# Kernel tuning notes

Hardware: AMD Instinct MI355X
Metric: run time of the kernel (lower is better)

The kernel has to match this reference:

```python
import jax, jax.numpy as jnp
import numpy as np
from jax.ops import segment_sum

N_NODES = 100000
N_EDGES = 3200000
DIM = 256
N_CLASSES = 32
N_GRAPHS = 64


def setup_inputs() -> dict:
    key = jax.random.key(0)
    k1, k2, k3, k4, k5 = jax.random.split(key, 5)
    x = jax.random.normal(k1, (N_NODES, DIM), dtype=jnp.float32)
    W = jax.random.normal(k2, (DIM, N_CLASSES), dtype=jnp.float32) / np.sqrt(DIM)
    b = jax.random.normal(k3, (N_CLASSES,), dtype=jnp.float32) * 0.01
    edge_index = jax.random.randint(k4, (2, N_EDGES), 0, N_NODES, dtype=jnp.int64)
    batch = jnp.sort(jax.random.randint(k5, (N_NODES,), 0, N_GRAPHS, dtype=jnp.int64))
    return {"x": x, "W": W, "b": b, "edge_index": edge_index, "batch": batch}


def reference(x, W, b, edge_index, batch):
    N = x.shape[0]
    # GCNConv: linear transform (no bias), then normalized aggregation, then bias
    h = x @ W  # [N, C]
    # add self loops (PyG default add_self_loops=True)
    loop = jnp.arange(N, dtype=edge_index.dtype)
    src = jnp.concatenate([edge_index[0], loop])  # source (message sender)
    dst = jnp.concatenate([edge_index[1], loop])  # target (aggregation site)
    # symmetric normalization: deg computed at target with unit edge weights
    deg = segment_sum(jnp.ones_like(dst, dtype=h.dtype), dst, num_segments=N)
    dinv = jnp.where(deg > 0, jax.lax.rsqrt(deg), 0.0)
    norm = dinv[src] * dinv[dst]  # [E+N]
    msg = h[src] * norm[:, None]  # gather + scale
    out = segment_sum(msg, dst, num_segments=N) + b  # scatter-add, bias after agg
    # global_mean_pool: segment mean over graphs
    cnt = segment_sum(jnp.ones((N,), dtype=out.dtype), batch, num_segments=N_GRAPHS)
    sums = segment_sum(out, batch, num_segments=N_GRAPHS)
    return sums / jnp.maximum(cnt, 1.0)[:, None]
```

## Files before the change

### kernel.cpp

```cpp
#include <hip/hip_runtime.h>

#define NN    100000
#define NE    3200000
#define DIMK  256
#define NC    32
#define NG    64

#define ROWS   64
#define NBUCK  1563
#define CAP    2432
#define NB1    512
#define EPB    6250
#define NSL    16
#define MAXG   512

static constexpr size_t OFF_REC    = 0;
static constexpr size_t OFF_DINV   = 15204864;
static constexpr size_t OFF_BTOT   = 15604864;
static constexpr size_t OFF_START  = 15613056;
static constexpr size_t OFF_CTRL   = 15613568;
static constexpr size_t OFF_P2     = 15613696;
static constexpr size_t OFF_PART   = 16662272;
static constexpr size_t OFF_DEGARR = OFF_PART;
static constexpr size_t OFF_CNT    = OFF_PART + 400000;
static constexpr size_t OFF_EXC    = OFF_PART + 3601024;

__device__ __forceinline__ int idx_at(const void* p, long i, bool i64) {
    return i64 ? (int)((const long long*)p)[i] : ((const int*)p)[i];
}

__device__ __forceinline__ bool detect_i64(const void* ei) {
    const int* w = (const int*)ei;
    return (w[1] == 0) & (w[3] == 0) & (w[5] == 0) &
           (w[7] == 0) & (w[9] == 0) & (w[11] == 0);
}

__global__ __launch_bounds__(256) void k_pre(const void* __restrict__ ei,
        unsigned int* __restrict__ parts, int* __restrict__ cnt) {
    __shared__ unsigned int h[12500];
    const bool i64 = detect_i64(ei);
    const int b = blockIdx.x;
    if (b < 256) {
        const int hh = b >> 7;
        const int sl = b & 127;
        const int lo = hh * 50000, hi = lo + 50000;
        for (int t = threadIdx.x; t < 12500; t += 256) h[t] = 0u;
        __syncthreads();
        const int e0 = sl * 25000;
        for (int e = e0 + threadIdx.x; e < e0 + 25000; e += 256) {
            int d = idx_at(ei, (long)NE + e, i64);
            if (d >= lo && d < hi) {
                int r = d - lo;
                atomicAdd(&h[r >> 2], 1u << ((r & 3) * 8));
            }
        }
        __syncthreads();
        for (int t = threadIdx.x; t < 12500; t += 256)
            parts[(size_t)b * 12500 + t] = h[t];
    } else {
        const int k = b - 256;
        for (int t = threadIdx.x; t < NBUCK; t += 256) h[t] = 0u;
        __syncthreads();
        const int e0 = k * EPB;
        for (int e = e0 + threadIdx.x; e < e0 + EPB; e += 256) {
            int s = idx_at(ei, e, i64);
            atomicAdd(&h[s >> 6], 1u);
        }
        __syncthreads();
        for (int t = threadIdx.x; t < NBUCK; t += 256)
            cnt[t * NB1 + k] = (int)h[t];
    }
}

__global__ __launch_bounds__(512) void k_mid(const unsigned int* __restrict__ parts,
        unsigned int* __restrict__ degarr, float* __restrict__ dinv,
        const void* __restrict__ batch, const void* __restrict__ ei,
        int* __restrict__ start, const int* __restrict__ cnt,
        int* __restrict__ exc, int* __restrict__ btot) {
    __shared__ int s[512];
    const int b = blockIdx.x;
    const int t = threadIdx.x;
    if (b < 49) {
        int i = b * 512 + t;
        if (i >= 25000) return;
        int h = (i >= 12500) ? 1 : 0;
        int w = i - h * 12500;
        int c0 = 0, c1 = 0, c2 = 0, c3 = 0;
        const unsigned int* base = parts + (size_t)(h * 128) * 12500 + w;
#pragma unroll 4
        for (int q = 0; q < 128; ++q) {
            unsigned int v = base[(size_t)q * 12500];
            c0 += v & 255u; c1 += (v >> 8) & 255u; c2 += (v >> 16) & 255u; c3 += v >> 24;
        }
        int node = h * 50000 + w * 4;
        degarr[node]     = 1u + c0;  dinv[node]     = 1.0f / sqrtf((float)(1 + c0));
        degarr[node + 1] = 1u + c1;  dinv[node + 1] = 1.0f / sqrtf((float)(1 + c1));
        degarr[node + 2] = 1u + c2;  dinv[node + 2] = 1.0f / sqrtf((float)(1 + c2));
        degarr[node + 3] = 1u + c3;  dinv[node + 3] = 1.0f / sqrtf((float)(1 + c3));
    } else if (b < 245) {
        const bool i64 = detect_i64(ei);
        int i = (b - 49) * 512 + t;
        if (i >= NN) return;
        int bi = idx_at(batch, i, i64);
        int bp = (i == 0) ? -1 : idx_at(batch, i - 1, i64);
        for (int g = bp + 1; g <= bi; ++g) start[g] = i;
        if (i == NN - 1)
            for (int g = bi + 1; g <= NG; ++g) start[g] = NN;
    } else {
        const int bkt = b - 245;
        int v = cnt[bkt * NB1 + t];
        s[t] = v;
        __syncthreads();
        for (int off = 1; off < 512; off <<= 1) {
            int u = (t >= off) ? s[t - off] : 0;
            __syncthreads();
            s[t] += u;
            __syncthreads();
        }
        exc[bkt * NB1 + t] = bkt * CAP + (s[t] - v);
        if (t == 511) btot[bkt] = s[511];
    }
}

__global__ __launch_bounds__(256) void k_place(const void* __restrict__ ei,
        const void* __restrict__ batch, const unsigned int* __restrict__ degarr,
        const int* __restrict__ exc, unsigned int* __restrict__ rec,
        int* __restrict__ ctrl) {
    __shared__ unsigned int lc[NBUCK];
    __shared__ int lbase[NBUCK];
    const bool i64 = detect_i64(ei);
    const int k = blockIdx.x;
    if (k == 0 && threadIdx.x == 0) ctrl[1] = 0;
    for (int t = threadIdx.x; t < NBUCK; t += 256) {
        lc[t] = 0u;
        lbase[t] = exc[t * NB1 + k];
    }
    __syncthreads();
    const int e0 = k * EPB;
    for (int e = e0 + threadIdx.x; e < e0 + EPB; e += 256) {
        int s = idx_at(ei, e, i64);
        int d = idx_at(ei, (long)NE + e, i64);
        int g = idx_at(batch, d, i64);
        unsigned int deg = min(degarr[d], 1048575u);
        int b = s >> 6;
        unsigned int r = atomicAdd(&lc[b], 1u);
        rec[lbase[b] + (int)r] = (deg << 12) | (unsigned)(g * 64 + (s & 63));
    }
}

__global__ __launch_bounds__(512, 2) void k_fused(
        const float* __restrict__ x, const float* __restrict__ dinv,
        const void* __restrict__ batch, const void* __restrict__ ei,
        const unsigned int* __restrict__ rec, const int* __restrict__ btot,
        float* __restrict__ part, int* __restrict__ ctrl) {
    __shared__ __align__(16) float Ach[64 * ROWS];
    __shared__ __align__(16) float4 xs[2][512];
    __shared__ int sbkt;
    const bool i64 = detect_i64(ei);
    const int tid  = threadIdx.x;
    const int gi   = tid >> 6;
    const int lane = tid & 63;

    float acc[8][4];
#pragma unroll
    for (int g = 0; g < 8; ++g)
#pragma unroll
        for (int d = 0; d < 4; ++d) acc[g][d] = 0.0f;

    const float4* x4 = (const float4*)x;
    float4* Ach4 = (float4*)Ach;
    const float4 z4 = make_float4(0.f, 0.f, 0.f, 0.f);
    const int jmax = NN - 1;

    for (;;) {
        if (tid == 0) sbkt = atomicAdd(&ctrl[1], 1);
        __syncthreads();
        const int bkt = sbkt;
        if (bkt >= NBUCK) break;
        const int j0 = bkt * ROWS;

        Ach4[tid] = z4;
        Ach4[tid + 512] = z4;
        __syncthreads();
        if (tid < ROWS) {
            int j = j0 + tid;
            if (j < NN) Ach[idx_at(batch, j, i64) * 64 + tid] = dinv[j];
        }
        __syncthreads();
        {
            const int rb = bkt * CAP;
            const int re = rb + btot[bkt];
            for (int r = rb + tid; r < re; r += 512) {
                unsigned int q = rec[r];
                float val = 1.0f / sqrtf((float)(q >> 12));
                atomicAdd(&Ach[q & 4095u], val);
            }
        }
        __syncthreads();
        float areg[8];
        {
            float dv = dinv[min(j0 + lane, jmax)];
#pragma unroll
            for (int q = 0; q < 8; ++q)
                areg[q] = Ach[(gi * 8 + q) * 64 + lane] * dv;
        }
        {
            float4 pf = x4[(size_t)min(j0 + gi, jmax) * 64 + lane];
            xs[0][tid] = pf;
        }
        __syncthreads();

#pragma unroll
        for (int c = 0; c < 8; ++c) {
            const int nr = (c < 7) ? (c + 1) * 8 + 0 : 56;
            float4 pn = x4[(size_t)min(j0 + nr + gi, jmax) * 64 + lane];
            const float4* xr = xs[c & 1];
#pragma unroll
            for (int jj = 0; jj < 8; ++jj) {
                float4 xv = xr[jj * 64 + lane];
#pragma unroll
                for (int q = 0; q < 8; ++q) {
                    float aq = __int_as_float(__builtin_amdgcn_readlane(
                        __float_as_int(areg[q]), c * 8 + jj));
                    acc[q][0] = fmaf(aq, xv.x, acc[q][0]);
                    acc[q][1] = fmaf(aq, xv.y, acc[q][1]);
                    acc[q][2] = fmaf(aq, xv.z, acc[q][2]);
                    acc[q][3] = fmaf(aq, xv.w, acc[q][3]);
                }
            }
            xs[(c + 1) & 1][tid] = pn;
            __syncthreads();
        }
    }

    float* p = part + (size_t)blockIdx.x * (NG * DIMK);
#pragma unroll
    for (int g = 0; g < 8; ++g) {
        float4 w = make_float4(acc[g][0], acc[g][1], acc[g][2], acc[g][3]);
        ((float4*)(p + (gi * 8 + g) * DIMK))[lane] = w;
    }
}

__global__ __launch_bounds__(256) void k_reduce1(const float4* __restrict__ part,
        float4* __restrict__ p2, int nblk) {
    int id = blockIdx.x * 256 + threadIdx.x;
    int c4 = id & 4095;
    int sl = id >> 12;
    int span = (nblk + NSL - 1) / NSL;
    int b0 = sl * span, b1 = min(b0 + span, nblk);
    float4 s = make_float4(0.f, 0.f, 0.f, 0.f);
    for (int b = b0; b < b1; ++b) {
        float4 v = part[(size_t)b * 4096 + c4];
        s.x += v.x; s.y += v.y; s.z += v.z; s.w += v.w;
    }
    p2[(size_t)sl * 4096 + c4] = s;
}

__global__ __launch_bounds__(256) void k_final(const float* __restrict__ p2,
        const float* __restrict__ W, const float* __restrict__ bias,
        const int* __restrict__ start, float* __restrict__ out) {
    __shared__ float Sb[8 * DIMK];
    const int tid = threadIdx.x, b = blockIdx.x;
    for (int t = tid; t < 8 * DIMK; t += 256) {
        int gl = t >> 8, d = t & 255;
        float s = 0.f;
#pragma unroll
        for (int sl = 0; sl < NSL; ++sl)
            s += p2[(size_t)sl * (NG * DIMK) + (b * 8 + gl) * DIMK + d];
        Sb[t] = s;
    }
    __syncthreads();
    int g = tid >> 5, c = tid & 31;
    float sum = 0.f;
#pragma unroll 8
    for (int d = 0; d < DIMK; ++d)
        sum = fmaf(Sb[g * DIMK + d], W[d * NC + c], sum);
    int gg = b * 8 + g;
    float cn = (float)max(start[gg + 1] - start[gg], 1);
    out[gg * NC + c] = sum / cn + bias[c];
}

extern "C" void kernel_launch(void* const* d_in, const int* in_sizes, int n_in,
                              void* d_out, int out_size, void* d_ws, size_t ws_size,
                              hipStream_t stream) {
    const float* x    = (const float*)d_in[0];
    const float* W    = (const float*)d_in[1];
    const float* bias = (const float*)d_in[2];
    const void*  ei   = d_in[3];
    const void*  batch= d_in[4];
    float* out = (float*)d_out;

    char* ws = (char*)d_ws;
    unsigned int* rec  = (unsigned int*)(ws + OFF_REC);
    unsigned int* degp = (unsigned int*)(ws + OFF_REC);
    float* dinv  = (float*)(ws + OFF_DINV);
    int*   btot  = (int*)(ws + OFF_BTOT);
    int*   start = (int*)(ws + OFF_START);
    int*   ctrl  = (int*)(ws + OFF_CTRL);
    float* p2    = (float*)(ws + OFF_P2);
    float* part  = (float*)(ws + OFF_PART);
    unsigned int* degarr = (unsigned int*)(ws + OFF_DEGARR);
    int*   cnt   = (int*)(ws + OFF_CNT);
    int*   exc   = (int*)(ws + OFF_EXC);

    long avail = (long)(ws_size - OFF_PART) / 65536;
    int grid = (int)avail;
    if (grid > MAXG) grid = MAXG;
    if (grid < 64) grid = 64;

    k_pre    <<<768, 256, 0, stream>>>(ei, degp, cnt);
    k_mid    <<<1808, 512, 0, stream>>>(degp, degarr, dinv, batch, ei, start,
                                        cnt, exc, btot);
    k_place  <<<NB1, 256, 0, stream>>>(ei, batch, degarr, exc, rec, ctrl);
    k_fused  <<<grid, 512, 0, stream>>>(x, dinv, batch, ei, rec, btot, part, ctrl);
    k_reduce1<<<256, 256, 0, stream>>>((const float4*)part, (float4*)p2, grid);
    k_final  <<<8, 256, 0, stream>>>(p2, W, bias, start, out);
}
```

Before: 222.9 us.

## Use direct global-to-LDS loads with 16-row stages and merge reduction kernels

The x-tile staging in the fused kernel now uses global_load_lds to copy rows straight into shared memory instead of going through registers. Stages are widened from 8 to 16 rows, which halves the number of barriers per 64-row bucket and doubles the LDS buffer size. The two-kernel partial reduction plus final projection is replaced by a single 64-block tail kernel that sums all per-block partials directly, removing one launch and the intermediate buffer. The tail now reads the partials serially over up to 512 blocks per thread, and whether the async LDS loads complete before the barrier depends on how the compiler inserts waits for them.

```diff
diff --git a/kernel.cpp b/kernel.cpp
--- a/kernel.cpp
+++ b/kernel.cpp
@@ -11,7 +11,6 @@
 #define CAP    2432
 #define NB1    512
 #define EPB    6250
-#define NSL    16
 #define MAXG   512
 
 static constexpr size_t OFF_REC    = 0;
@@ -33,6 +32,12 @@
     const int* w = (const int*)ei;
     return (w[1] == 0) & (w[3] == 0) & (w[5] == 0) &
            (w[7] == 0) & (w[9] == 0) & (w[11] == 0);
+}
+
+__device__ __forceinline__ void gload16(const float4* g, float4* l) {
+    __builtin_amdgcn_global_load_lds(
+        (const __attribute__((address_space(1))) unsigned int*)g,
+        (__attribute__((address_space(3))) unsigned int*)l, 16, 0, 0);
 }
 
 __global__ __launch_bounds__(256) void k_pre(const void* __restrict__ ei,
@@ -154,7 +159,7 @@
         const unsigned int* __restrict__ rec, const int* __restrict__ btot,
         float* __restrict__ part, int* __restrict__ ctrl) {
     __shared__ __align__(16) float Ach[64 * ROWS];
-    __shared__ __align__(16) float4 xs[2][512];
+    __shared__ __align__(16) float4 xs[2][16 * 64];
     __shared__ int sbkt;
     const bool i64 = detect_i64(ei);
     const int tid  = threadIdx.x;
@@ -204,31 +209,37 @@
             for (int q = 0; q < 8; ++q)
                 areg[q] = Ach[(gi * 8 + q) * 64 + lane] * dv;
         }
-        {
-            float4 pf = x4[(size_t)min(j0 + gi, jmax) * 64 + lane];
-            xs[0][tid] = pf;
-        }
-        __syncthreads();
-
-#pragma unroll
-        for (int c = 0; c < 8; ++c) {
-            const int nr = (c < 7) ? (c + 1) * 8 + 0 : 56;
-            float4 pn = x4[(size_t)min(j0 + nr + gi, jmax) * 64 + lane];
+#pragma unroll
+        for (int r = 0; r < 2; ++r) {
+            int row = 2 * gi + r;
+            gload16(x4 + (size_t)min(j0 + row, jmax) * 64 + lane,
+                    &xs[0][row * 64]);
+        }
+        __syncthreads();
+
+#pragma unroll
+        for (int c = 0; c < 4; ++c) {
+            const int cn = (c < 3) ? c + 1 : 3;
+#pragma unroll
+            for (int r = 0; r < 2; ++r) {
+                int row = 2 * gi + r;
+                gload16(x4 + (size_t)min(j0 + cn * 16 + row, jmax) * 64 + lane,
+                        &xs[(c + 1) & 1][row * 64]);
+            }
             const float4* xr = xs[c & 1];
 #pragma unroll
-            for (int jj = 0; jj < 8; ++jj) {
+            for (int jj = 0; jj < 16; ++jj) {
                 float4 xv = xr[jj * 64 + lane];
 #pragma unroll
                 for (int q = 0; q < 8; ++q) {
                     float aq = __int_as_float(__builtin_amdgcn_readlane(
-                        __float_as_int(areg[q]), c * 8 + jj));
+                        __float_as_int(areg[q]), c * 16 + jj));
                     acc[q][0] = fmaf(aq, xv.x, acc[q][0]);
                     acc[q][1] = fmaf(aq, xv.y, acc[q][1]);
                     acc[q][2] = fmaf(aq, xv.z, acc[q][2]);
                     acc[q][3] = fmaf(aq, xv.w, acc[q][3]);
                 }
             }
-            xs[(c + 1) & 1][tid] = pn;
             __syncthreads();
         }
     }
@@ -241,43 +252,26 @@
     }
 }
 
-__global__ __launch_bounds__(256) void k_reduce1(const float4* __restrict__ part,
-        float4* __restrict__ p2, int nblk) {
-    int id = blockIdx.x * 256 + threadIdx.x;
-    int c4 = id & 4095;
-    int sl = id >> 12;
-    int span = (nblk + NSL - 1) / NSL;
-    int b0 = sl * span, b1 = min(b0 + span, nblk);
-    float4 s = make_float4(0.f, 0.f, 0.f, 0.f);
-    for (int b = b0; b < b1; ++b) {
-        float4 v = part[(size_t)b * 4096 + c4];
-        s.x += v.x; s.y += v.y; s.z += v.z; s.w += v.w;
-    }
-    p2[(size_t)sl * 4096 + c4] = s;
-}
-
-__global__ __launch_bounds__(256) void k_final(const float* __restrict__ p2,
+__global__ __launch_bounds__(256) void k_tail(const float* __restrict__ part,
         const float* __restrict__ W, const float* __restrict__ bias,
-        const int* __restrict__ start, float* __restrict__ out) {
-    __shared__ float Sb[8 * DIMK];
-    const int tid = threadIdx.x, b = blockIdx.x;
-    for (int t = tid; t < 8 * DIMK; t += 256) {
-        int gl = t >> 8, d = t & 255;
-        float s = 0.f;
-#pragma unroll
-        for (int sl = 0; sl < NSL; ++sl)
-            s += p2[(size_t)sl * (NG * DIMK) + (b * 8 + gl) * DIMK + d];
-        Sb[t] = s;
-    }
+        const int* __restrict__ start, float* __restrict__ out, int nblk) {
+    __shared__ float Sb[DIMK];
+    const int tid = threadIdx.x, g = blockIdx.x;
+    float s = 0.f;
+    const float* p = part + g * DIMK + tid;
+#pragma unroll 4
+    for (int b = 0; b < nblk; ++b)
+        s += p[(size_t)b * (NG * DIMK)];
+    Sb[tid] = s;
     __syncthreads();
-    int g = tid >> 5, c = tid & 31;
-    float sum = 0.f;
+    if (tid < NC) {
+        float sum = 0.f;
 #pragma unroll 8
-    for (int d = 0; d < DIMK; ++d)
-        sum = fmaf(Sb[g * DIMK + d], W[d * NC + c], sum);
-    int gg = b * 8 + g;
-    float cn = (float)max(start[gg + 1] - start[gg], 1);
-    out[gg * NC + c] = sum / cn + bias[c];
+        for (int d = 0; d < DIMK; ++d)
+            sum = fmaf(Sb[d], W[d * NC + tid], sum);
+        float cn = (float)max(start[g + 1] - start[g], 1);
+        out[g * NC + tid] = sum / cn + bias[tid];
+    }
 }
 
 extern "C" void kernel_launch(void* const* d_in, const int* in_sizes, int n_in,
@@ -297,7 +291,6 @@
     int*   btot  = (int*)(ws + OFF_BTOT);
     int*   start = (int*)(ws + OFF_START);
     int*   ctrl  = (int*)(ws + OFF_CTRL);
-    float* p2    = (float*)(ws + OFF_P2);
     float* part  = (float*)(ws + OFF_PART);
     unsigned int* degarr = (unsigned int*)(ws + OFF_DEGARR);
     int*   cnt   = (int*)(ws + OFF_CNT);
@@ -308,11 +301,10 @@
     if (grid > MAXG) grid = MAXG;
     if (grid < 64) grid = 64;
 
-    k_pre    <<<768, 256, 0, stream>>>(ei, degp, cnt);
-    k_mid    <<<1808, 512, 0, stream>>>(degp, degarr, dinv, batch, ei, start,
-                                        cnt, exc, btot);
-    k_place  <<<NB1, 256, 0, stream>>>(ei, batch, degarr, exc, rec, ctrl);
-    k_fused  <<<grid, 512, 0, stream>>>(x, dinv, batch, ei, rec, btot, part, ctrl);
-    k_reduce1<<<256, 256, 0, stream>>>((const float4*)part, (float4*)p2, grid);
-    k_final  <<<8, 256, 0, stream>>>(p2, W, bias, start, out);
-}
+    k_pre  <<<768, 256, 0, stream>>>(ei, degp, cnt);
+    k_mid  <<<1808, 512, 0, stream>>>(degp, degarr, dinv, batch, ei, start,
+                                      cnt, exc, btot);
+    k_place<<<NB1, 256, 0, stream>>>(ei, batch, degarr, exc, rec, ctrl);
+    k_fused<<<grid, 512, 0, stream>>>(x, dinv, batch, ei, rec, btot, part, ctrl);
+    k_tail <<<NG, 256, 0, stream>>>(part, W, bias, start, out, grid);
+}
```

Result: slower. 239.4 us (+7.4%).
